# Optimization experiments

Measured on AMD Instinct MI355X. Metric: run time of the kernel, lower is better.

The kernel has to match this reference:

```python
import jax, jax.numpy as jnp
import numpy as np


def setup_inputs() -> dict:
    key = jax.random.key(0)
    k1, k2 = jax.random.split(key)
    B, G, N, C = 32, 64, 32, 3  # batch, num point groups, points per group, xyz
    xyz1_matrix = jax.random.normal(k1, (B, G, N, C), dtype=jnp.float32)
    xyz2_matrix = jax.random.normal(k2, (B, G, N, C), dtype=jnp.float32)
    return {"xyz1_matrix": xyz1_matrix, "xyz2_matrix": xyz2_matrix}


def reference(xyz1_matrix, xyz2_matrix):
    # xyz1_matrix: [B, G1, N1, 3], xyz2_matrix: [B, G2, N2, 3]
    # Pairwise squared L2 distances between every point of every group in set 1
    x2 = jnp.sum(xyz1_matrix * xyz1_matrix, axis=-1)  # [B, G1, N1]
    y2 = jnp.sum(xyz2_matrix * xyz2_matrix, axis=-1)  # [B, G2, N2]
    cross = jnp.einsum('bgnc,bhmc->bghnm', xyz1_matrix, xyz2_matrix)  # [B,G1,G2,N1,N2]
    d = x2[:, :, None, :, None] + y2[:, None, :, None, :] - 2.0 * cross
    # Nearest-neighbor (min over the other cloud) for both directions.
    dist1 = jnp.min(d, axis=-1)  # [B, G1, G2, N1]: for each pt in group g1, nearest in g2
    dist2 = jnp.min(d, axis=-2)  # [B, G1, G2, N2]: for each pt in group g2, nearest in g1
    # (dist2 here already corresponds to the torch dist2.permute(0, 2, 1, 3).)
    return jnp.mean(dist1, axis=-1) + jnp.mean(dist2, axis=-1)  # [B, G1, G2]
```

## Files before the change

### kernel.cpp

```cpp
#include <hip/hip_runtime.h>


__global__ __launch_bounds__(256, 4)
void chamfer_dist_kernel(const float* __restrict__ xyz1,
                         const float* __restrict__ xyz2,
                         float* __restrict__ out) {
    const int b    = blockIdx.x >> 5;
    const int pair = blockIdx.x & 31;
    const int wave = threadIdx.x >> 6;
    const int lane = threadIdx.x & 63;
    const int g1   = (pair << 1) | (wave >> 1);
    const int g2   = ((wave & 1) << 5) | (lane & 31);
    const int half = lane >> 5;

    const float* __restrict__ p2 =
        xyz2 + (size_t)(b * 64 + g2) * 96 + half * 48;
    const float4* __restrict__ p2v = reinterpret_cast<const float4*>(p2);

    float qx[16], qy[16], qz[16], s2[16], colmin[16];
#pragma unroll
    for (int i = 0; i < 4; ++i) {
        const float4 va = p2v[3 * i + 0];
        const float4 vb = p2v[3 * i + 1];
        const float4 vc = p2v[3 * i + 2];
        const float f[12] = {va.x, va.y, va.z, va.w,
                             vb.x, vb.y, vb.z, vb.w,
                             vc.x, vc.y, vc.z, vc.w};
#pragma unroll
        for (int j = 0; j < 4; ++j) {
            const int m = 4 * i + j;
            const float x = f[3 * j + 0];
            const float y = f[3 * j + 1];
            const float z = f[3 * j + 2];
            s2[m] = fmaf(x, x, fmaf(y, y, z * z));
            qx[m] = -2.0f * x;
            qy[m] = -2.0f * y;
            qz[m] = -2.0f * z;
            colmin[m] = 3.0e38f;
        }
    }

    const int off1 = __builtin_amdgcn_readfirstlane((b * 64 + g1) * 96);
    const float* __restrict__ p1 = xyz1 + off1;

    float sum1 = 0.0f;

#pragma unroll 4
    for (int n = 0; n < 32; ++n) {
        const float x1 = p1[3 * n + 0];
        const float y1 = p1[3 * n + 1];
        const float z1 = p1[3 * n + 2];
        const float s1 = fmaf(x1, x1, fmaf(y1, y1, z1 * z1));
        float rmin = 3.0e38f;
#pragma unroll
        for (int m = 0; m < 16; m += 2) {
            const float t0 = fmaf(x1, qx[m],
                             fmaf(y1, qy[m],
                             fmaf(z1, qz[m], s1 + s2[m])));
            const float t1 = fmaf(x1, qx[m + 1],
                             fmaf(y1, qy[m + 1],
                             fmaf(z1, qz[m + 1], s1 + s2[m + 1])));
            rmin = fminf(fminf(t0, t1), rmin);
            colmin[m]     = fminf(colmin[m], t0);
            colmin[m + 1] = fminf(colmin[m + 1], t1);
        }
        rmin = fminf(rmin, __shfl_xor(rmin, 32, 64));
        sum1 += rmin;
    }

    float sum2 = 0.0f;
#pragma unroll
    for (int m = 0; m < 16; ++m) sum2 += colmin[m];
    sum2 += __shfl_xor(sum2, 32, 64);

    if (half == 0)
        out[(size_t)(b * 64 + g1) * 64 + g2] = (sum1 + sum2) * (1.0f / 32.0f);
}

extern "C" void kernel_launch(void* const* d_in, const int* in_sizes, int n_in,
                              void* d_out, int out_size, void* d_ws, size_t ws_size,
                              hipStream_t stream) {
    const float* xyz1 = (const float*)d_in[0];
    const float* xyz2 = (const float*)d_in[1];
    float* out = (float*)d_out;

    dim3 grid(1024);
    dim3 block(256);
    chamfer_dist_kernel<<<grid, block, 0, stream>>>(xyz1, xyz2, out);
}
```

Baseline: 73.49 us.

## Assign one full (g1,g2) pair per lane and process two query points per iteration

Each thread now holds all 32 points of its g2 group instead of splitting them across two half-waves, which removes the cross-half shuffle for the row minimum and the idle half-wave at the store. The inner loop handles two xyz1 points per iteration and moves the s1 addition out of the FMA chain, adding it only for the column-min update and the final row sum. The grid is halved and launch bounds relaxed to 2 blocks per CU to make room for the doubled register arrays. The cost is higher register pressure and fewer waves available to hide latency.

```diff
diff --git a/kernel.cpp b/kernel.cpp
--- a/kernel.cpp
+++ b/kernel.cpp
@@ -1,25 +1,20 @@
 #include <hip/hip_runtime.h>
 
 
-__global__ __launch_bounds__(256, 4)
+__global__ __launch_bounds__(256, 2)
 void chamfer_dist_kernel(const float* __restrict__ xyz1,
                          const float* __restrict__ xyz2,
                          float* __restrict__ out) {
-    const int b    = blockIdx.x >> 5;
-    const int pair = blockIdx.x & 31;
-    const int wave = threadIdx.x >> 6;
-    const int lane = threadIdx.x & 63;
-    const int g1   = (pair << 1) | (wave >> 1);
-    const int g2   = ((wave & 1) << 5) | (lane & 31);
-    const int half = lane >> 5;
+    const int b  = blockIdx.x >> 4;
+    const int g1 = ((blockIdx.x & 15) << 2) | (threadIdx.x >> 6);
+    const int g2 = threadIdx.x & 63;
 
-    const float* __restrict__ p2 =
-        xyz2 + (size_t)(b * 64 + g2) * 96 + half * 48;
-    const float4* __restrict__ p2v = reinterpret_cast<const float4*>(p2);
+    const float4* __restrict__ p2v =
+        reinterpret_cast<const float4*>(xyz2 + (size_t)(b * 64 + g2) * 96);
 
-    float qx[16], qy[16], qz[16], s2[16], colmin[16];
+    float qx[32], qy[32], qz[32], s2[32], colmin[32];
 #pragma unroll
-    for (int i = 0; i < 4; ++i) {
+    for (int i = 0; i < 8; ++i) {
         const float4 va = p2v[3 * i + 0];
         const float4 vb = p2v[3 * i + 1];
         const float4 vc = p2v[3 * i + 2];
@@ -45,36 +40,36 @@
 
     float sum1 = 0.0f;
 
-#pragma unroll 4
-    for (int n = 0; n < 32; ++n) {
-        const float x1 = p1[3 * n + 0];
-        const float y1 = p1[3 * n + 1];
-        const float z1 = p1[3 * n + 2];
-        const float s1 = fmaf(x1, x1, fmaf(y1, y1, z1 * z1));
-        float rmin = 3.0e38f;
+#pragma unroll 2
+    for (int n = 0; n < 32; n += 2) {
+        const float xa = p1[3 * n + 0];
+        const float ya = p1[3 * n + 1];
+        const float za = p1[3 * n + 2];
+        const float xb = p1[3 * n + 3];
+        const float yb = p1[3 * n + 4];
+        const float zb = p1[3 * n + 5];
+        const float s1a = fmaf(xa, xa, fmaf(ya, ya, za * za));
+        const float s1b = fmaf(xb, xb, fmaf(yb, yb, zb * zb));
+        float ra = 3.0e38f, rb = 3.0e38f;
 #pragma unroll
-        for (int m = 0; m < 16; m += 2) {
-            const float t0 = fmaf(x1, qx[m],
-                             fmaf(y1, qy[m],
-                             fmaf(z1, qz[m], s1 + s2[m])));
-            const float t1 = fmaf(x1, qx[m + 1],
-                             fmaf(y1, qy[m + 1],
-                             fmaf(z1, qz[m + 1], s1 + s2[m + 1])));
-            rmin = fminf(fminf(t0, t1), rmin);
-            colmin[m]     = fminf(colmin[m], t0);
-            colmin[m + 1] = fminf(colmin[m + 1], t1);
+        for (int m = 0; m < 32; m += 2) {
+            const float t00 = fmaf(xa, qx[m    ], fmaf(ya, qy[m    ], fmaf(za, qz[m    ], s2[m    ])));
+            const float t01 = fmaf(xa, qx[m + 1], fmaf(ya, qy[m + 1], fmaf(za, qz[m + 1], s2[m + 1])));
+            const float t10 = fmaf(xb, qx[m    ], fmaf(yb, qy[m    ], fmaf(zb, qz[m    ], s2[m    ])));
+            const float t11 = fmaf(xb, qx[m + 1], fmaf(yb, qy[m + 1], fmaf(zb, qz[m + 1], s2[m + 1])));
+            ra = fminf(fminf(t00, t01), ra);
+            rb = fminf(fminf(t10, t11), rb);
+            colmin[m    ] = fminf(fminf(t00 + s1a, t10 + s1b), colmin[m    ]);
+            colmin[m + 1] = fminf(fminf(t01 + s1a, t11 + s1b), colmin[m + 1]);
         }
-        rmin = fminf(rmin, __shfl_xor(rmin, 32, 64));
-        sum1 += rmin;
+        sum1 += (s1a + ra) + (s1b + rb);
     }
 
     float sum2 = 0.0f;
 #pragma unroll
-    for (int m = 0; m < 16; ++m) sum2 += colmin[m];
-    sum2 += __shfl_xor(sum2, 32, 64);
+    for (int m = 0; m < 32; ++m) sum2 += colmin[m];
 
-    if (half == 0)
-        out[(size_t)(b * 64 + g1) * 64 + g2] = (sum1 + sum2) * (1.0f / 32.0f);
+    out[(size_t)(b * 64 + g1) * 64 + g2] = (sum1 + sum2) * (1.0f / 32.0f);
 }
 
 extern "C" void kernel_launch(void* const* d_in, const int* in_sizes, int n_in,
@@ -84,7 +79,7 @@
     const float* xyz2 = (const float*)d_in[1];
     float* out = (float*)d_out;
 
-    dim3 grid(1024);
+    dim3 grid(512);
     dim3 block(256);
     chamfer_dist_kernel<<<grid, block, 0, stream>>>(xyz1, xyz2, out);
 }
```

Measured after the change: 77.04 us. 1.05x slower.

## Hoist row norm out of inner loop, process point pairs, prefetch xyz1 as float4

Applied to the files above, without the earlier changes.

The inner distance computation drops the per-point s1 addition from the row-min path. s1 is added once after the row minimum is taken, and added to the column-min candidates only where needed. Points from set 1 are now handled two at a time, sharing the loaded qx/qy/qz/s2 operands. The xyz1 rows are read with software-prefetched float4 vector loads instead of scalar loads. The aim is fewer VALU instructions and less load latency in the hot loop, at the cost of more live registers and a changed floating-point rounding order.

```diff
diff --git a/kernel.cpp b/kernel.cpp
--- a/kernel.cpp
+++ b/kernel.cpp
@@ -13,9 +13,8 @@
     const int g2   = ((wave & 1) << 5) | (lane & 31);
     const int half = lane >> 5;
 
-    const float* __restrict__ p2 =
-        xyz2 + (size_t)(b * 64 + g2) * 96 + half * 48;
-    const float4* __restrict__ p2v = reinterpret_cast<const float4*>(p2);
+    const float4* __restrict__ p2v = reinterpret_cast<const float4*>(
+        xyz2 + (size_t)(b * 64 + g2) * 96 + half * 48);
 
     float qx[16], qy[16], qz[16], s2[16], colmin[16];
 #pragma unroll
@@ -40,32 +39,44 @@
         }
     }
 
-    const int off1 = __builtin_amdgcn_readfirstlane((b * 64 + g1) * 96);
-    const float* __restrict__ p1 = xyz1 + off1;
-
     float sum1 = 0.0f;
 
-#pragma unroll 4
-    for (int n = 0; n < 32; ++n) {
-        const float x1 = p1[3 * n + 0];
-        const float y1 = p1[3 * n + 1];
-        const float z1 = p1[3 * n + 2];
-        const float s1 = fmaf(x1, x1, fmaf(y1, y1, z1 * z1));
-        float rmin = 3.0e38f;
+    auto npair = [&](float xa, float ya, float za,
+                     float xb, float yb, float zb) {
+        const float s1a = fmaf(xa, xa, fmaf(ya, ya, za * za));
+        const float s1b = fmaf(xb, xb, fmaf(yb, yb, zb * zb));
+        float ra = 3.0e38f, rb = 3.0e38f;
 #pragma unroll
         for (int m = 0; m < 16; m += 2) {
-            const float t0 = fmaf(x1, qx[m],
-                             fmaf(y1, qy[m],
-                             fmaf(z1, qz[m], s1 + s2[m])));
-            const float t1 = fmaf(x1, qx[m + 1],
-                             fmaf(y1, qy[m + 1],
-                             fmaf(z1, qz[m + 1], s1 + s2[m + 1])));
-            rmin = fminf(fminf(t0, t1), rmin);
-            colmin[m]     = fminf(colmin[m], t0);
-            colmin[m + 1] = fminf(colmin[m + 1], t1);
+            const float t00 = fmaf(xa, qx[m    ], fmaf(ya, qy[m    ], fmaf(za, qz[m    ], s2[m    ])));
+            const float t01 = fmaf(xa, qx[m + 1], fmaf(ya, qy[m + 1], fmaf(za, qz[m + 1], s2[m + 1])));
+            const float t10 = fmaf(xb, qx[m    ], fmaf(yb, qy[m    ], fmaf(zb, qz[m    ], s2[m    ])));
+            const float t11 = fmaf(xb, qx[m + 1], fmaf(yb, qy[m + 1], fmaf(zb, qz[m + 1], s2[m + 1])));
+            ra = fminf(fminf(t00, t01), ra);
+            rb = fminf(fminf(t10, t11), rb);
+            colmin[m    ] = fminf(fminf(t00 + s1a, t10 + s1b), colmin[m    ]);
+            colmin[m + 1] = fminf(fminf(t01 + s1a, t11 + s1b), colmin[m + 1]);
         }
-        rmin = fminf(rmin, __shfl_xor(rmin, 32, 64));
-        sum1 += rmin;
+        ra = fminf(ra, __shfl_xor(ra, 32, 64));
+        rb = fminf(rb, __shfl_xor(rb, 32, 64));
+        sum1 += (s1a + ra) + (s1b + rb);
+    };
+
+    const float4* __restrict__ p1v = reinterpret_cast<const float4*>(
+        xyz1 + (size_t)(b * 64 + g1) * 96);
+
+    float4 A0 = p1v[0], A1 = p1v[1], A2 = p1v[2];
+#pragma unroll
+    for (int c = 0; c < 8; ++c) {
+        float4 B0, B1, B2;
+        if (c < 7) {
+            B0 = p1v[3 * c + 3];
+            B1 = p1v[3 * c + 4];
+            B2 = p1v[3 * c + 5];
+        }
+        npair(A0.x, A0.y, A0.z, A0.w, A1.x, A1.y);
+        npair(A1.z, A1.w, A2.x, A2.y, A2.z, A2.w);
+        if (c < 7) { A0 = B0; A1 = B1; A2 = B2; }
     }
 
     float sum2 = 0.0f;
```

Measured after the change: 130.9 us. 78.1% more time.
